# Optimization experiments

Hardware: AMD Instinct MI355X
Metric: run time of the kernel (lower is better)

The kernel has to match this reference:

```python
import jax, jax.numpy as jnp
import numpy as np

NUM_EXPERTS = 16
TOP_K = 2
FFT_LEN = 512
SEQ_LEN = 512
PRED_LEN = 720
MOE_TEMP = 1.0


def setup_inputs() -> dict:
    key = jax.random.key(0)
    ks = jax.random.split(key, 5)
    x = jax.random.normal(ks[0], (8192, SEQ_LEN), dtype=jnp.float32)
    # gating network: Linear(fft_len//2 -> num_experts)
    gw = jax.random.normal(ks[1], (NUM_EXPERTS, FFT_LEN // 2), dtype=jnp.float32) * (1.0 / np.sqrt(FFT_LEN // 2))
    gb = jnp.zeros((NUM_EXPERTS,), dtype=jnp.float32)
    # experts: RLinear = instance-norm (RevIN) + Linear(seq->pred), stacked
    ew = jax.random.normal(ks[2], (NUM_EXPERTS, SEQ_LEN, PRED_LEN), dtype=jnp.float32) * (1.0 / np.sqrt(SEQ_LEN))
    eb = jnp.zeros((NUM_EXPERTS, PRED_LEN), dtype=jnp.float32)
    return {"x": x, "gw": gw, "gb": gb, "ew": ew, "eb": eb}


def periodogram(x, n):
    # x: [B, L] -> normalized power spectrum [B, n//2]
    x0 = x - jnp.mean(x, axis=1, keepdims=True)
    dft = jnp.fft.fft(x0, n=n, axis=1) / jnp.sqrt(jnp.asarray(n, x.dtype))
    I = jnp.abs(dft[:, : n // 2]) ** 2
    s = jnp.sum(I, axis=1, keepdims=True)
    s = jnp.where(s == 0, 1.0, s)
    return I / s


def expert_apply(x, ew, eb):
    # RLinear: instance normalize, linear map, de-normalize
    mu = jnp.mean(x, axis=1, keepdims=True)
    sd = jnp.std(x, axis=1, keepdims=True) + 1e-5
    xn = (x - mu) / sd  # [B, L]
    # all experts densely: [B,L] x [E,L,P] -> [E,B,P]
    y = jnp.einsum('bl,elp->ebp', xn, ew) + eb[:, None, :]
    return y * sd[None] + mu[None]  # [E, B, P]


def reference(x, gw, gb, ew, eb):
    I = periodogram(x, FFT_LEN)  # [B, n//2]
    gate = (I @ gw.T + gb) / MOE_TEMP  # eval mode: divide by temp, no noise
    topk_vals, topk_idx = jax.lax.top_k(gate, TOP_K)  # [B, k]
    gates = jax.nn.softmax(topk_vals, axis=1)  # [B, k]
    expert_out = expert_apply(x, ew, eb)  # [E, B, P]
    # gather selected experts: [B, k, P]
    sel = jnp.take_along_axis(
        jnp.transpose(expert_out, (1, 0, 2)), topk_idx[:, :, None], axis=1
    )
    return jnp.sum(gates[:, :, None] * sel, axis=1)  # [B, P]
```

## Files before the change

kernel.cpp:

```cpp
#include <hip/hip_runtime.h>
#include <hip/hip_bf16.h>
#include <math.h>

#define NEXP  16
#define SEQ   512
#define PRED  720
#define NROWS 8192
#define NFREQ 256

typedef __bf16 bf16x8 __attribute__((ext_vector_type(8)));
typedef float  f32x16 __attribute__((ext_vector_type(16)));

__device__ __forceinline__ void gload_lds16(const void* g, void* l) {
    __builtin_amdgcn_global_load_lds(
        (const __attribute__((address_space(1))) unsigned int*)g,
        (__attribute__((address_space(3))) unsigned int*)l, 16, 0, 0);
}

__device__ __forceinline__ int xcd_swizzle(int bid, int nwg) {
    const int q = nwg >> 3, r = nwg & 7;
    const int xcd = bid & 7, off = bid >> 3;
    return (xcd < r ? xcd * (q + 1) : r * (q + 1) + (xcd - r) * q) + off;
}

__global__ __launch_bounds__(256) void k_preproc(const float* __restrict__ ew,
                                                 const float* __restrict__ x,
                                                 __hip_bfloat16* __restrict__ ewt,
                                                 __hip_bfloat16* __restrict__ bthi,
                                                 __hip_bfloat16* __restrict__ btlo,
                                                 __hip_bfloat16* __restrict__ xn,
                                                 __hip_bfloat16* __restrict__ xnlo,
                                                 float* __restrict__ meta,
                                                 int* __restrict__ nredo)
{
    const int bid = blockIdx.x;
    const int t   = threadIdx.x;

    if (bid < 512) {
        if (bid == 0 && t == 0) *nredo = 0;
        const int tid  = bid * 256 + t;
        const int f    = tid >> 9;
        const int lidx = tid & 511;
        const int m    = (f * lidx) & 511;

        constexpr double Cj[9] = {0.9999247018391445033, 0.9996988186962042201,
                                  0.9987954562051723927, 0.9951847266721968862,
                                  0.9807852804032304491, 0.9238795325112867561,
                                  0.7071067811865475244, 0.0, -1.0};
        constexpr double Sj[9] = {0.0122715382857199261, 0.0245412285229122880,
                                  0.0490676743274180143, 0.0980171403295606020,
                                  0.1950903220161282678, 0.3826834323650897717,
                                  0.7071067811865475244, 1.0, 0.0};
        double cr = 1.0, ci = 0.0;
#pragma unroll
        for (int j = 0; j < 9; ++j) {
            const bool on = (m >> j) & 1;
            const double mr = on ? Cj[j] : 1.0;
            const double mi = on ? Sj[j] : 0.0;
            const double nr = cr * mr - ci * mi;
            ci = cr * mi + ci * mr;
            cr = nr;
        }
        const size_t c0 = (size_t)(2 * f) * 512 + lidx;
        const size_t c1 = (size_t)(2 * f + 1) * 512 + lidx;
        {
            __hip_bfloat16 h = __float2bfloat16((float)cr);
            float hif = __bfloat162float(h);
            bthi[c0] = h;
            btlo[c0] = __float2bfloat16((float)(cr - (double)hif));
        }
        {
            __hip_bfloat16 h = __float2bfloat16((float)ci);
            float hif = __bfloat162float(h);
            bthi[c1] = h;
            btlo[c1] = __float2bfloat16((float)(ci - (double)hif));
        }
        return;
    }

    if (bid < 6400) {
        __shared__ float tile[32][33];
        const int rel = bid - 512;
        const int e   = rel / 368;
        const int rem = rel % 368;
        const int p0  = (rem % 23) * 32;
        const int l0  = (rem / 23) * 32;
        const int tx  = t & 31;
        const int ty  = t >> 5;
        const float* src = ew + (size_t)e * SEQ * PRED;
#pragma unroll
        for (int i = 0; i < 4; ++i) {
            int l = l0 + ty + i * 8;
            int p = p0 + tx;
            tile[ty + i * 8][tx] = (p < PRED) ? src[(size_t)l * PRED + p] : 0.f;
        }
        __syncthreads();
        __hip_bfloat16* dst = ewt + (size_t)e * PRED * SEQ;
#pragma unroll
        for (int i = 0; i < 4; ++i) {
            int p = p0 + ty + i * 8;
            int l = l0 + tx;
            if (p < PRED) dst[(size_t)p * SEQ + l] = __float2bfloat16(tile[tx][ty + i * 8]);
        }
        return;
    }

    {
        const int wv = t >> 6, l = t & 63;
        const int b  = (bid - 6400) * 4 + wv;
        const float* xr = x + (size_t)b * SEQ;

        const float4 v0 = *(const float4*)(xr + l * 8);
        const float4 v1 = *(const float4*)(xr + l * 8 + 4);
        const double d0 = v0.x, d1 = v0.y, d2 = v0.z, d3 = v0.w;
        const double d4 = v1.x, d5 = v1.y, d6 = v1.z, d7 = v1.w;

        double s1 = ((d0 + d1) + (d2 + d3)) + ((d4 + d5) + (d6 + d7));
        double s2 = ((d0 * d0 + d1 * d1) + (d2 * d2 + d3 * d3)) +
                    ((d4 * d4 + d5 * d5) + (d6 * d6 + d7 * d7));
#pragma unroll
        for (int off = 1; off < 64; off <<= 1) {
            s1 += __shfl_xor(s1, off);
            s2 += __shfl_xor(s2, off);
        }
        const double mu = s1 * (1.0 / 512.0);
        double var = s2 * (1.0 / 512.0) - mu * mu;
        if (var < 0.0) var = 0.0;
        const double sd = sqrt(var) + 1e-5, inv = 1.0 / sd;

        unsigned int hw[4], lw[4];
#define CONV(j, dj)                                                         \
        {                                                                   \
            double xnd = (dj - mu) * inv;                                   \
            __hip_bfloat16 h = __float2bfloat16((float)xnd);                \
            float hif = __bfloat162float(h);                                \
            __hip_bfloat16 lo = __float2bfloat16((float)(xnd - (double)hif)); \
            unsigned int hb = *(unsigned short*)&h;                         \
            unsigned int lb = *(unsigned short*)&lo;                        \
            if ((j & 1) == 0) { hw[j >> 1] = hb; lw[j >> 1] = lb; }         \
            else { hw[j >> 1] |= hb << 16; lw[j >> 1] |= lb << 16; }        \
        }
        CONV(0, d0) CONV(1, d1) CONV(2, d2) CONV(3, d3)
        CONV(4, d4) CONV(5, d5) CONV(6, d6) CONV(7, d7)
#undef CONV
        *(uint4*)(xn   + (size_t)b * SEQ + l * 8) = uint4{hw[0], hw[1], hw[2], hw[3]};
        *(uint4*)(xnlo + (size_t)b * SEQ + l * 8) = uint4{lw[0], lw[1], lw[2], lw[3]};

        if (l == 0) {
            meta[b * 4 + 0] = (float)mu;
            meta[b * 4 + 3] = (float)sd;
        }
    }
}

__global__ __launch_bounds__(256, 3) void k_dft_gemm(
    const __hip_bfloat16* __restrict__ xn, const __hip_bfloat16* __restrict__ xnlo,
    const __hip_bfloat16* __restrict__ bthi, const __hip_bfloat16* __restrict__ btlo,
    float* __restrict__ Iout)
{
    const int wgid = xcd_swizzle(blockIdx.x, 1024);
    const int rt = wgid >> 3;
    const int ct = wgid & 7;

    __shared__ __align__(16) __hip_bfloat16 As[3][64][64];
    __shared__ __align__(16) __hip_bfloat16 Bs[3][64][64];

    const int t  = threadIdx.x;
    const int wv = t >> 6, l = t & 63;

    size_t aoff[2], boff[2];
    int ldsrow[2], ldschk[2];
#pragma unroll
    for (int i = 0; i < 2; ++i) {
        const int idx = i * 256 + t;
        const int row = idx >> 3, chk = idx & 7;
        const int swz = (row & 7) ^ ((row & 8) >> 1);
        ldsrow[i] = row; ldschk[i] = chk;
        aoff[i] = (size_t)(rt * 64 + row) * SEQ + (size_t)(chk ^ swz) * 8;
        boff[i] = (size_t)(ct * 64 + row) * SEQ + (size_t)(chk ^ swz) * 8;
    }

#define DSTAGE(buf, kk) do {                                                   \
    const int pass_ = (kk) >> 3;                                               \
    const int koff_ = ((kk) & 7) * 64;                                         \
    const __hip_bfloat16* ap_ = (pass_ == 1) ? xnlo : xn;                      \
    const __hip_bfloat16* bp_ = (pass_ == 2) ? btlo : bthi;                    \
    _Pragma("unroll")                                                          \
    for (int i_ = 0; i_ < 2; ++i_)                                             \
        gload_lds16(ap_ + aoff[i_] + koff_, &As[buf][ldsrow[i_]][ldschk[i_] * 8]); \
    _Pragma("unroll")                                                          \
    for (int i_ = 0; i_ < 2; ++i_)                                             \
        gload_lds16(bp_ + boff[i_] + koff_, &Bs[buf][ldsrow[i_]][ldschk[i_] * 8]); \
} while (0)

    f32x16 acc;
#pragma unroll
    for (int q = 0; q < 16; ++q) acc[q] = 0.f;

    const int wr = wv >> 1, wc = wv & 1;
    const int fl = l & 31, fh = l >> 5;
    const int rswz = (fl & 7) ^ ((fl & 8) >> 1);

    DSTAGE(0, 0);
    DSTAGE(1, 1);
#pragma unroll
    for (int kt = 0; kt < 24; ++kt) {
        const int cur = kt % 3;
        if (kt < 23) asm volatile("s_waitcnt vmcnt(4)" ::: "memory");
        else         asm volatile("s_waitcnt vmcnt(0)" ::: "memory");
        __builtin_amdgcn_sched_barrier(0);
        __builtin_amdgcn_s_barrier();
        __builtin_amdgcn_sched_barrier(0);
#pragma unroll
        for (int ks = 0; ks < 4; ++ks) {
            const int cc = ((ks * 2 + fh) ^ rswz) * 8;
            const bf16x8 a = *(const bf16x8*)&As[cur][wr * 32 + fl][cc];
            const bf16x8 b = *(const bf16x8*)&Bs[cur][wc * 32 + fl][cc];
            acc = __builtin_amdgcn_mfma_f32_32x32x16_bf16(a, b, acc, 0, 0, 0);
        }
        if (kt + 2 < 24) DSTAGE((kt + 2) % 3, kt + 2);
    }
#undef DSTAGE

    const int crow_base = 4 * fh;
    const int col = ct * 64 + wc * 32 + fl;
#pragma unroll
    for (int q = 0; q < 16; ++q) {
        const float v = acc[q];
        const float w = __shfl_xor(v, 1);
        if ((fl & 1) == 0) {
            const int rl = wr * 32 + (q & 3) + 8 * (q >> 2) + crow_base;
            Iout[(size_t)(rt * 64 + rl) * NFREQ + (col >> 1)] = v * v + w * w;
        }
    }
}

__global__ __launch_bounds__(256) void k_gatefin(const float* __restrict__ Iout,
                                                 const float* __restrict__ gw,
                                                 const float* __restrict__ gb,
                                                 float* __restrict__ meta,
                                                 int* __restrict__ eidx,
                                                 int* __restrict__ redo,
                                                 int* __restrict__ nredo)
{
    __shared__ float gws[NEXP * 257];
    __shared__ float Pw[4][256];
    __shared__ float Gs[4][16];

    const int t  = threadIdx.x;
    const int wv = t >> 6, l = t & 63;
    const int b  = blockIdx.x * 4 + wv;

    for (int i = t; i < NEXP * NFREQ; i += 256)
        gws[(i >> 8) * 257 + (i & 255)] = gw[i];
    __syncthreads();

    const float* Ir = Iout + (size_t)b * NFREQ;
    const float i0 = Ir[l], i1 = Ir[64 + l], i2 = Ir[128 + l], i3 = Ir[192 + l];
    Pw[wv][l] = i0; Pw[wv][64 + l] = i1; Pw[wv][128 + l] = i2; Pw[wv][192 + l] = i3;
    float ps = (i0 + i1) + (i2 + i3);
#pragma unroll
    for (int off = 1; off < 64; off <<= 1) ps += __shfl_xor(ps, off);

    const int e = l >> 2, kb = l & 3;
    float acc = 0.f;
#pragma unroll 8
    for (int j = 0; j < 64; ++j) {
        const int k = kb + 4 * j;
        acc += Pw[wv][k] * gws[e * 257 + k];
    }
    acc += __shfl_xor(acc, 1);
    acc += __shfl_xor(acc, 2);
    if (kb == 0) Gs[wv][e] = acc;

    if (l == 0) {
        const float sdiv  = (ps == 0.f) ? 1.f : ps;
        const float inv_s = 1.f / sdiv;
        float b1 = -1e30f, b2 = -1e30f, b3 = -1e30f;
        int i1b = 0, i2b = 0;
#pragma unroll
        for (int i = 0; i < NEXP; ++i) {
            float v = Gs[wv][i] * inv_s + gb[i];
            if (v > b1)      { b3 = b2; b2 = b1; i2b = i1b; b1 = v; i1b = i; }
            else if (v > b2) { b3 = b2; b2 = v; i2b = i; }
            else if (v > b3) { b3 = v; }
        }
        if (b2 - b3 < 1e-4f * fmaxf(1.f, fabsf(b1))) {
            const int r = atomicAdd(nredo, 1);
            redo[r] = b;
        } else {
            const float sd = meta[b * 4 + 3];
            const float ee = __expf(b2 - b1);
            const float w0 = 1.f / (1.f + ee);
            const float w1 = ee / (1.f + ee);
            meta[b * 4 + 1] = w0 * sd;
            meta[b * 4 + 2] = w1 * sd;
            eidx[b * 2 + 0] = i1b;
            eidx[b * 2 + 1] = i2b;
        }
    }
}

__global__ __launch_bounds__(256, 4) void k_gate64(const float* __restrict__ x,
                                                   const float* __restrict__ gw,
                                                   const float* __restrict__ gb,
                                                   float* __restrict__ meta,
                                                   int* __restrict__ eidx,
                                                   const int* __restrict__ redo,
                                                   const int* __restrict__ nredo)
{
    __shared__ double Pw[4][256];
    __shared__ double Gs[4][16];

    const int t  = threadIdx.x;
    const int wv = t >> 6, l = t & 63;
    const int n  = *nredo;

    for (int it = blockIdx.x * 4 + wv; it < n; it += gridDim.x * 4) {
        const int b = redo[it];
        const float* xr = x + (size_t)b * SEQ;

        double s1 = 0.0, s2 = 0.0;
#define DLOADV(n_) double vr##n_ = (double)xr[64 * n_ + l]; s1 += vr##n_; s2 += vr##n_ * vr##n_;
        DLOADV(0) DLOADV(1) DLOADV(2) DLOADV(3) DLOADV(4) DLOADV(5) DLOADV(6) DLOADV(7)
#undef DLOADV
        double vi0, vi1, vi2, vi3, vi4, vi5, vi6, vi7;

#pragma unroll
        for (int off = 1; off < 64; off <<= 1) {
            s1 += __shfl_xor(s1, off);
            s2 += __shfl_xor(s2, off);
        }
        const double mu = s1 * (1.0 / 512.0);
        double var = s2 * (1.0 / 512.0) - mu * mu;
        if (var < 0.0) var = 0.0;
        const double sd = sqrt(var) + 1e-5;

#define DSUB(n_) vr##n_ -= mu;
        DSUB(0) DSUB(1) DSUB(2) DSUB(3) DSUB(4) DSUB(5) DSUB(6) DSUB(7)
#undef DSUB

        {
            const double C = 0.70710678118654752440084436210485;
            double a0 = vr0 + vr4, a1 = vr1 + vr5, a2 = vr2 + vr6, a3 = vr3 + vr7;
            double d0 = vr0 - vr4, d1 = vr1 - vr5, d2 = vr2 - vr6, d3 = vr3 - vr7;
            double c0 = a0 + a2, c2 = a0 - a2, c1 = a1 + a3;
            double c3i = a3 - a1;
            double e1r = C * (d1 - d3), e1i = -C * (d1 + d3);
            vr0 = c0 + c1;   vi0 = 0.0;
            vr1 = c0 - c1;   vi1 = 0.0;
            vr2 = c2;        vi2 = c3i;
            vr3 = c2;        vi3 = -c3i;
            vr4 = d0 + e1r;  vi4 = -d2 + e1i;
            vr5 = d0 - e1r;  vi5 = -d2 - e1i;
            vr6 = d0 - e1r;  vi6 =  d2 + e1i;
            vr7 = d0 + e1r;  vi7 =  d2 - e1i;
        }

        double w1r = 1.0, w1i = 0.0;
        {
            constexpr double Cr[6] = {0.9999247018391445033, 0.9996988186962042201,
                                      0.9987954562051723927, 0.9951847266721968862,
                                      0.9807852804032304491, 0.9238795325112867561};
            constexpr double Ci[6] = {-0.0122715382857199261, -0.0245412285229122880,
                                      -0.0490676743274180143, -0.0980171403295606020,
                                      -0.1950903220161282678, -0.3826834323650897717};
#pragma unroll
            for (int j = 0; j < 6; ++j) {
                const bool on = (l >> j) & 1;
                const double mr = on ? Cr[j] : 1.0;
                const double mi = on ? Ci[j] : 0.0;
                const double nr = w1r * mr - w1i * mi;
                w1i = w1r * mi + w1i * mr;
                w1r = nr;
            }
        }

        {
            double wkr = w1r, wki = w1i;
#define DTWID(n_) { double tr_ = vr##n_ * wkr - vi##n_ * wki; \
                    vi##n_ = vr##n_ * wki + vi##n_ * wkr; vr##n_ = tr_; }
#define DWSTEP() { double nr_ = wkr * w1r - wki * w1i; \
                   wki = wkr * w1i + wki * w1r; wkr = nr_; }
            DTWID(4) DWSTEP() DTWID(2) DWSTEP() DTWID(6) DWSTEP() DTWID(1)
            DWSTEP() DTWID(5) DWSTEP() DTWID(3) DWSTEP() DTWID(7)
#undef DTWID
#undef DWSTEP
        }

        double twr, twi;
        {
            double w2r = w1r * w1r - w1i * w1i, w2i = 2.0 * w1r * w1i;
            double w4r = w2r * w2r - w2i * w2i, w4i = 2.0 * w2r * w2i;
            twr = w4r * w4r - w4i * w4i; twi = 2.0 * w4r * w4i;
        }
#define DBF(R, I, h, hi, ter, tei) { \
        double br_ = __shfl_xor(R, h); double bi_ = __shfl_xor(I, h); \
        double dr_ = hi ? (R - br_) : (R + br_); \
        double di_ = hi ? (I - bi_) : (I + bi_); \
        R = dr_ * ter - di_ * tei; I = dr_ * tei + di_ * ter; }
#define DSTG(hc) { \
        const bool hi_ = (l & hc) != 0; \
        const double ter_ = hi_ ? twr : 1.0; \
        const double tei_ = hi_ ? twi : 0.0; \
        DBF(vr0, vi0, hc, hi_, ter_, tei_) DBF(vr1, vi1, hc, hi_, ter_, tei_) \
        DBF(vr2, vi2, hc, hi_, ter_, tei_) DBF(vr3, vi3, hc, hi_, ter_, tei_) \
        DBF(vr4, vi4, hc, hi_, ter_, tei_) DBF(vr5, vi5, hc, hi_, ter_, tei_) \
        DBF(vr6, vi6, hc, hi_, ter_, tei_) DBF(vr7, vi7, hc, hi_, ter_, tei_) \
        double ntr_ = twr * twr - twi * twi; twi = 2.0 * twr * twi; twr = ntr_; }
        DSTG(32) DSTG(16) DSTG(8) DSTG(4) DSTG(2) DSTG(1)
#undef DSTG
#undef DBF

        const int k2 = (int)(__brev((unsigned)l) >> 26);
        double ps = 0.0;
        if ((l & 1) == 0) {
            const int kb = 8 * k2;
            double P;
            P = vr0 * vr0 + vi0 * vi0; ps += P; Pw[wv][0 + kb] = P;
            P = vr1 * vr1 + vi1 * vi1; ps += P; Pw[wv][4 + kb] = P;
            P = vr2 * vr2 + vi2 * vi2; ps += P; Pw[wv][2 + kb] = P;
            P = vr3 * vr3 + vi3 * vi3; ps += P; Pw[wv][6 + kb] = P;
            P = vr4 * vr4 + vi4 * vi4; ps += P; Pw[wv][1 + kb] = P;
            P = vr5 * vr5 + vi5 * vi5; ps += P; Pw[wv][5 + kb] = P;
            P = vr6 * vr6 + vi6 * vi6; ps += P; Pw[wv][3 + kb] = P;
            P = vr7 * vr7 + vi7 * vi7; ps += P; Pw[wv][7 + kb] = P;
        }
#pragma unroll
        for (int off = 1; off < 64; off <<= 1) ps += __shfl_xor(ps, off);

        {
            const int e = l >> 2, kb = l & 3;
            double acc = 0.0;
#pragma unroll 8
            for (int j = 0; j < 64; ++j) {
                int k = kb + 4 * j;
                acc += Pw[wv][k] * (double)gw[e * NFREQ + k];
            }
            acc += __shfl_xor(acc, 1);
            acc += __shfl_xor(acc, 2);
            if (kb == 0) Gs[wv][e] = acc;
        }

        if (l == 0) {
            const double sdiv  = (ps == 0.0) ? 1.0 : ps;
            const double inv_s = 1.0 / sdiv;
            double best = -1e300, best2 = -1e300;
            int i0b = 0, i1b = 0;
#pragma unroll
            for (int i = 0; i < NEXP; ++i) {
                double v = Gs[wv][i] * inv_s + (double)gb[i];
                if (v > best)       { best2 = best; i1b = i0b; best = v; i0b = i; }
                else if (v > best2) { best2 = v; i1b = i; }
            }
            const double eexp = (double)__expf((float)(best2 - best));
            const double w0 = 1.0 / (1.0 + eexp);
            const double w1 = eexp / (1.0 + eexp);
            meta[b * 4 + 0] = (float)mu;
            meta[b * 4 + 1] = (float)(w0 * sd);
            meta[b * 4 + 2] = (float)(w1 * sd);
            meta[b * 4 + 3] = (float)sd;
            eidx[b * 2 + 0] = i0b;
            eidx[b * 2 + 1] = i1b;
        }
    }
}

__global__ __launch_bounds__(256) void k_count(const int* __restrict__ eidx,
                                               int* __restrict__ blockHist)
{
    __shared__ int h[32];
    const int t   = threadIdx.x;
    const int blk = blockIdx.x;
    if (t < 32) h[t] = 0;
    __syncthreads();
    const int b  = blk * 256 + t;
    const int e0 = eidx[2 * b];
    const int e1 = eidx[2 * b + 1];
    atomicAdd(&h[e0], 1);
    atomicAdd(&h[16 + e1], 1);
    __syncthreads();
    if (t < 32) blockHist[(t >> 4) * 512 + blk * 16 + (t & 15)] = h[t];
}

__global__ void k_scan(const int* __restrict__ blockHist, int* __restrict__ counts,
                       int* __restrict__ offs, int* __restrict__ tdesc,
                       int* __restrict__ base)
{
    __shared__ int cnt[32];
    __shared__ int off_s[32];
    const int j = threadIdx.x;
    if (j < 32) {
        const int s = j >> 4, e = j & 15;
        int acc = 0;
        for (int blk = 0; blk < 32; ++blk) acc += blockHist[s * 512 + blk * 16 + e];
        cnt[j] = acc;
        counts[j] = acc;
    }
    __syncthreads();
    if (j < 2) {
        int acc = 0, tt = 0;
        for (int i = 0; i < NEXP; ++i) {
            const int c = cnt[j * 16 + i];
            off_s[j * 16 + i] = acc;
            offs[j * 16 + i]  = acc;
            acc += c;
            const int nt = (c + 63) >> 6;
            for (int k = 0; k < nt; ++k) tdesc[j * 160 + tt++] = (i << 16) | k;
        }
        for (; tt < 160; ++tt) tdesc[j * 160 + tt] = -1;
    }
    __syncthreads();
    if (j < 32) {
        const int s = j >> 4, e = j & 15;
        int run = off_s[j];
        for (int blk = 0; blk < 32; ++blk) {
            base[s * 512 + blk * 16 + e] = run;
            run += blockHist[s * 512 + blk * 16 + e];
        }
    }
}

__global__ __launch_bounds__(256) void k_scatter(const int* __restrict__ eidx,
                                                 const int* __restrict__ base,
                                                 int* __restrict__ lists)
{
    __shared__ int whist[2][4][16];
    const int t   = threadIdx.x;
    const int wv  = t >> 6, l = t & 63;
    const int blk = blockIdx.x;
    const int b   = blk * 256 + t;
    const int e0  = eidx[2 * b];
    const int e1  = eidx[2 * b + 1];
    const unsigned long long before = (1ULL << l) - 1ULL;

    unsigned long long m0 = 0, m1 = 0;
#pragma unroll
    for (int bb = 0; bb < 16; ++bb) {
        unsigned long long m = __ballot(e0 == bb);
        if (e0 == bb) m0 = m;
        if (l == 0) whist[0][wv][bb] = __popcll(m);
    }
#pragma unroll
    for (int bb = 0; bb < 16; ++bb) {
        unsigned long long m = __ballot(e1 == bb);
        if (e1 == bb) m1 = m;
        if (l == 0) whist[1][wv][bb] = __popcll(m);
    }
    __syncthreads();

    int p0 = __popcll(m0 & before);
    int p1 = __popcll(m1 & before);
    for (int w = 0; w < 4; ++w) {
        if (w < wv) {
            p0 += whist[0][w][e0];
            p1 += whist[1][w][e1];
        }
    }
    lists[base[blk * 16 + e0] + p0]                 = b;
    lists[NROWS + base[512 + blk * 16 + e1] + p1]   = b;
}

__global__ __launch_bounds__(256, 3) void k_expert_gemm(
    const __hip_bfloat16* __restrict__ xn, const __hip_bfloat16* __restrict__ ewt,
    const float* __restrict__ eb, const float* __restrict__ meta,
    const int* __restrict__ lists, const int* __restrict__ offs,
    const int* __restrict__ counts, const int* __restrict__ tdesc,
    float* __restrict__ out, float* __restrict__ out2)
{
    const int wgid = xcd_swizzle(blockIdx.x, 3456);
    const int slot = wgid / 1728;
    const int rem  = wgid - slot * 1728;
    const int tid  = rem / 12;
    const int ct   = rem % 12;
    const int d    = tdesc[slot * 160 + tid];
    if (d < 0) return;
    const int e  = d >> 16;
    const int rt = d & 0xffff;
    const int n_e = counts[slot * NEXP + e];

    __shared__ __align__(16) __hip_bfloat16 As[3][64][64];
    __shared__ __align__(16) __hip_bfloat16 Bs[3][64][64];
    __shared__ int   rowB[64];
    __shared__ float rowMu[64];
    __shared__ float rowC[64];

    const int t  = threadIdx.x;
    const int wv = t >> 6, l = t & 63;
    const int* list = lists + slot * NROWS + offs[slot * NEXP + e];
    if (t < 64) {
        int r  = rt * 64 + t;
        int bb = (r < n_e) ? list[r] : -1;
        rowB[t]  = bb;
        rowMu[t] = (bb >= 0) ? meta[bb * 4] : 0.f;
        rowC[t]  = (bb >= 0) ? meta[bb * 4 + 1 + slot] : 0.f;
    }
    __syncthreads();

    const __hip_bfloat16* asrc[2];
    const __hip_bfloat16* bsrc[2];
    int ldsrow[2], ldschk[2];
#pragma unroll
    for (int i = 0; i < 2; ++i) {
        const int idx = i * 256 + t;
        const int row = idx >> 3, chk = idx & 7;
        const int swz = (row & 7) ^ ((row & 8) >> 1);
        ldsrow[i] = row; ldschk[i] = chk;
        const int ab  = rowB[row];
        asrc[i] = xn + ((ab >= 0) ? (size_t)ab * SEQ : 0) + (size_t)(chk ^ swz) * 8;
        const int gc  = ct * 64 + row;
        const int gcc = (gc < PRED) ? gc : (PRED - 1);
        bsrc[i] = ewt + ((size_t)e * PRED + gcc) * SEQ + (size_t)(chk ^ swz) * 8;
    }

#define STAGE(buf, koff) do {                                                      \
    _Pragma("unroll")                                                              \
    for (int i_ = 0; i_ < 2; ++i_)                                                 \
        gload_lds16(asrc[i_] + (koff), &As[buf][ldsrow[i_]][ldschk[i_] * 8]);      \
    _Pragma("unroll")                                                              \
    for (int i_ = 0; i_ < 2; ++i_)                                                 \
        gload_lds16(bsrc[i_] + (koff), &Bs[buf][ldsrow[i_]][ldschk[i_] * 8]);      \
} while (0)

    f32x16 acc;
#pragma unroll
    for (int q = 0; q < 16; ++q) acc[q] = 0.f;

    const int wr = wv >> 1, wc = wv & 1;
    const int fl = l & 31, fh = l >> 5;
    const int rswz = (fl & 7) ^ ((fl & 8) >> 1);

    STAGE(0, 0);
    STAGE(1, 64);
#pragma unroll
    for (int kt = 0; kt < 8; ++kt) {
        const int cur = kt % 3;
        if (kt < 7) asm volatile("s_waitcnt vmcnt(4)" ::: "memory");
        else        asm volatile("s_waitcnt vmcnt(0)" ::: "memory");
        __builtin_amdgcn_sched_barrier(0);
        __builtin_amdgcn_s_barrier();
        __builtin_amdgcn_sched_barrier(0);
#pragma unroll
        for (int ks = 0; ks < 4; ++ks) {
            const int cc = ((ks * 2 + fh) ^ rswz) * 8;
            const bf16x8 a = *(const bf16x8*)&As[cur][wr * 32 + fl][cc];
            const bf16x8 b = *(const bf16x8*)&Bs[cur][wc * 32 + fl][cc];
            acc = __builtin_amdgcn_mfma_f32_32x32x16_bf16(a, b, acc, 0, 0, 0);
        }
        if (kt + 2 < 8) STAGE((kt + 2) % 3, (kt + 2) * 64);
    }
#undef STAGE

    const int crow_base = 4 * fh;
    const int col = ct * 64 + wc * 32 + fl;
    const bool cok = (col < PRED);
    const float ebv = cok ? eb[e * PRED + col] : 0.f;
#pragma unroll
    for (int q = 0; q < 16; ++q) {
        const int rl = wr * 32 + (q & 3) + 8 * (q >> 2) + crow_base;
        const int bb = rowB[rl];
        if (!cok || bb < 0) continue;
        const float v = acc[q] + ebv;
        if (slot == 0) out [(size_t)bb * PRED + col] = rowMu[rl] + rowC[rl] * v;
        else           out2[(size_t)bb * PRED + col] = rowC[rl] * v;
    }
}

__global__ __launch_bounds__(256) void k_merge(float* __restrict__ out,
                                               const float* __restrict__ out2)
{
    const int i = blockIdx.x * 256 + threadIdx.x;
    float4 a = ((float4*)out)[i];
    const float4 b = ((const float4*)out2)[i];
    a.x += b.x; a.y += b.y; a.z += b.z; a.w += b.w;
    ((float4*)out)[i] = a;
}

extern "C" void kernel_launch(void* const* d_in, const int* in_sizes, int n_in,
                              void* d_out, int out_size, void* d_ws, size_t ws_size,
                              hipStream_t stream)
{
    const float* x  = (const float*)d_in[0];
    const float* gw = (const float*)d_in[1];
    const float* gb = (const float*)d_in[2];
    const float* ew = (const float*)d_in[3];
    const float* eb = (const float*)d_in[4];
    float* out = (float*)d_out;
    char*  ws  = (char*)d_ws;

    constexpr size_t XN_OFF   = 0;
    constexpr size_t XN_SZ    = (size_t)NROWS * SEQ * 2;
    constexpr size_t XNLO_OFF = XN_OFF + XN_SZ;
    constexpr size_t EWT_OFF  = XNLO_OFF + XN_SZ;
    constexpr size_t EWT_SZ   = (size_t)NEXP * PRED * SEQ * 2;
    constexpr size_t BTHI_OFF = EWT_OFF + EWT_SZ;
    constexpr size_t BT_SZ    = (size_t)512 * 512 * 2;
    constexpr size_t BTLO_OFF = BTHI_OFF + BT_SZ;
    constexpr size_t IOUT_OFF = BTLO_OFF + BT_SZ;
    constexpr size_t IOUT_SZ  = (size_t)NROWS * NFREQ * 4;
    constexpr size_t META_OFF = IOUT_OFF + IOUT_SZ;
    constexpr size_t META_SZ  = (size_t)NROWS * 4 * 4;
    constexpr size_t EIDX_OFF = META_OFF + META_SZ;
    constexpr size_t EIDX_SZ  = (size_t)NROWS * 2 * 4;
    constexpr size_t LIST_OFF = EIDX_OFF + EIDX_SZ;
    constexpr size_t LIST_SZ  = (size_t)2 * NROWS * 4;
    constexpr size_t CNT_OFF  = LIST_OFF + LIST_SZ;
    constexpr size_t OFFS_OFF = CNT_OFF + 144;
    constexpr size_t TDSC_OFF = OFFS_OFF + 128;
    constexpr size_t BH_OFF   = TDSC_OFF + 1280;
    constexpr size_t BASE_OFF = BH_OFF + 4096;
    constexpr size_t REDO_OFF = BASE_OFF + 4096;
    constexpr size_t OUT2_OFF = REDO_OFF + (size_t)NROWS * 4;

    __hip_bfloat16* xn   = (__hip_bfloat16*)(ws + XN_OFF);
    __hip_bfloat16* xnlo = (__hip_bfloat16*)(ws + XNLO_OFF);
    __hip_bfloat16* ewt  = (__hip_bfloat16*)(ws + EWT_OFF);
    __hip_bfloat16* bthi = (__hip_bfloat16*)(ws + BTHI_OFF);
    __hip_bfloat16* btlo = (__hip_bfloat16*)(ws + BTLO_OFF);
    float* Iout  = (float*)(ws + IOUT_OFF);
    float* meta  = (float*)(ws + META_OFF);
    int* eidx    = (int*)(ws + EIDX_OFF);
    int* lists   = (int*)(ws + LIST_OFF);
    int* counts  = (int*)(ws + CNT_OFF);
    int* nredo   = (int*)(ws + CNT_OFF + 128);
    int* offs    = (int*)(ws + OFFS_OFF);
    int* tdesc   = (int*)(ws + TDSC_OFF);
    int* bhist   = (int*)(ws + BH_OFF);
    int* base    = (int*)(ws + BASE_OFF);
    int* redo    = (int*)(ws + REDO_OFF);
    float* out2  = (float*)(ws + OUT2_OFF);

    k_preproc<<<dim3(8448), dim3(256), 0, stream>>>(ew, x, ewt, bthi, btlo,
                                                    xn, xnlo, meta, nredo);
    k_dft_gemm<<<dim3(1024), dim3(256), 0, stream>>>(xn, xnlo, bthi, btlo, Iout);
    k_gatefin<<<dim3(NROWS / 4), dim3(256), 0, stream>>>(Iout, gw, gb, meta, eidx,
                                                         redo, nredo);
    k_gate64<<<dim3(64), dim3(256), 0, stream>>>(x, gw, gb, meta, eidx, redo, nredo);
    k_count<<<dim3(32), dim3(256), 0, stream>>>(eidx, bhist);
    k_scan<<<dim3(1), dim3(64), 0, stream>>>(bhist, counts, offs, tdesc, base);
    k_scatter<<<dim3(32), dim3(256), 0, stream>>>(eidx, base, lists);
    k_expert_gemm<<<dim3(3456), dim3(256), 0, stream>>>(
        xn, ewt, eb, meta, lists, offs, counts, tdesc, out, out2);
    k_merge<<<dim3(NROWS * PRED / 1024), dim3(256), 0, stream>>>(out, out2);
}
```

Measured before the change: 141.7 us.

## Widen GEMM N-tiles to 128 with double buffering and MFMA priority boost

```diff
diff --git a/kernel.cpp b/kernel.cpp
--- a/kernel.cpp
+++ b/kernel.cpp
@@ -158,26 +158,33 @@
     const __hip_bfloat16* __restrict__ bthi, const __hip_bfloat16* __restrict__ btlo,
     float* __restrict__ Iout)
 {
-    const int wgid = xcd_swizzle(blockIdx.x, 1024);
-    const int rt = wgid >> 3;
-    const int ct = wgid & 7;
-
-    __shared__ __align__(16) __hip_bfloat16 As[3][64][64];
-    __shared__ __align__(16) __hip_bfloat16 Bs[3][64][64];
+    const int wgid = xcd_swizzle(blockIdx.x, 512);
+    const int rt = wgid >> 2;
+    const int ct = wgid & 3;
+
+    __shared__ __align__(16) __hip_bfloat16 As[2][64][64];
+    __shared__ __align__(16) __hip_bfloat16 Bs[2][128][64];
 
     const int t  = threadIdx.x;
     const int wv = t >> 6, l = t & 63;
 
-    size_t aoff[2], boff[2];
-    int ldsrow[2], ldschk[2];
+    size_t aoff[2], boff[4];
+    int arow[2], achk[2], brow[4], bchk[4];
 #pragma unroll
     for (int i = 0; i < 2; ++i) {
         const int idx = i * 256 + t;
         const int row = idx >> 3, chk = idx & 7;
         const int swz = (row & 7) ^ ((row & 8) >> 1);
-        ldsrow[i] = row; ldschk[i] = chk;
+        arow[i] = row; achk[i] = chk;
         aoff[i] = (size_t)(rt * 64 + row) * SEQ + (size_t)(chk ^ swz) * 8;
-        boff[i] = (size_t)(ct * 64 + row) * SEQ + (size_t)(chk ^ swz) * 8;
+    }
+#pragma unroll
+    for (int i = 0; i < 4; ++i) {
+        const int idx = i * 256 + t;
+        const int row = idx >> 3, chk = idx & 7;
+        const int swz = (row & 7) ^ ((row & 8) >> 1);
+        brow[i] = row; bchk[i] = chk;
+        boff[i] = (size_t)(ct * 128 + row) * SEQ + (size_t)(chk ^ swz) * 8;
     }
 
 #define DSTAGE(buf, kk) do {                                                   \
@@ -187,50 +194,59 @@
     const __hip_bfloat16* bp_ = (pass_ == 2) ? btlo : bthi;                    \
     _Pragma("unroll")                                                          \
     for (int i_ = 0; i_ < 2; ++i_)                                             \
-        gload_lds16(ap_ + aoff[i_] + koff_, &As[buf][ldsrow[i_]][ldschk[i_] * 8]); \
+        gload_lds16(ap_ + aoff[i_] + koff_, &As[buf][arow[i_]][achk[i_] * 8]); \
     _Pragma("unroll")                                                          \
-    for (int i_ = 0; i_ < 2; ++i_)                                             \
-        gload_lds16(bp_ + boff[i_] + koff_, &Bs[buf][ldsrow[i_]][ldschk[i_] * 8]); \
+    for (int i_ = 0; i_ < 4; ++i_)                                             \
+        gload_lds16(bp_ + boff[i_] + koff_, &Bs[buf][brow[i_]][bchk[i_] * 8]); \
 } while (0)
 
-    f32x16 acc;
-#pragma unroll
-    for (int q = 0; q < 16; ++q) acc[q] = 0.f;
+    f32x16 acc[2];
+#pragma unroll
+    for (int ni = 0; ni < 2; ++ni)
+#pragma unroll
+        for (int q = 0; q < 16; ++q) acc[ni][q] = 0.f;
 
     const int wr = wv >> 1, wc = wv & 1;
     const int fl = l & 31, fh = l >> 5;
     const int rswz = (fl & 7) ^ ((fl & 8) >> 1);
 
     DSTAGE(0, 0);
-    DSTAGE(1, 1);
+    asm volatile("s_waitcnt vmcnt(0)" ::: "memory");
+    __builtin_amdgcn_s_barrier();
 #pragma unroll
     for (int kt = 0; kt < 24; ++kt) {
-        const int cur = kt % 3;
-        if (kt < 23) asm volatile("s_waitcnt vmcnt(4)" ::: "memory");
-        else         asm volatile("s_waitcnt vmcnt(0)" ::: "memory");
+        const int cur = kt & 1;
+        if (kt < 23) DSTAGE(cur ^ 1, kt + 1);
         __builtin_amdgcn_sched_barrier(0);
-        __builtin_amdgcn_s_barrier();
-        __builtin_amdgcn_sched_barrier(0);
+        __builtin_amdgcn_s_setprio(1);
 #pragma unroll
         for (int ks = 0; ks < 4; ++ks) {
             const int cc = ((ks * 2 + fh) ^ rswz) * 8;
-            const bf16x8 a = *(const bf16x8*)&As[cur][wr * 32 + fl][cc];
-            const bf16x8 b = *(const bf16x8*)&Bs[cur][wc * 32 + fl][cc];
-            acc = __builtin_amdgcn_mfma_f32_32x32x16_bf16(a, b, acc, 0, 0, 0);
-        }
-        if (kt + 2 < 24) DSTAGE((kt + 2) % 3, kt + 2);
+            const bf16x8 a  = *(const bf16x8*)&As[cur][wr * 32 + fl][cc];
+            const bf16x8 b0 = *(const bf16x8*)&Bs[cur][wc * 64 + fl][cc];
+            const bf16x8 b1 = *(const bf16x8*)&Bs[cur][wc * 64 + 32 + fl][cc];
+            acc[0] = __builtin_amdgcn_mfma_f32_32x32x16_bf16(a, b0, acc[0], 0, 0, 0);
+            acc[1] = __builtin_amdgcn_mfma_f32_32x32x16_bf16(a, b1, acc[1], 0, 0, 0);
+        }
+        __builtin_amdgcn_s_setprio(0);
+        __builtin_amdgcn_sched_barrier(0);
+        asm volatile("s_waitcnt vmcnt(0)" ::: "memory");
+        __builtin_amdgcn_s_barrier();
     }
 #undef DSTAGE
 
     const int crow_base = 4 * fh;
-    const int col = ct * 64 + wc * 32 + fl;
-#pragma unroll
-    for (int q = 0; q < 16; ++q) {
-        const float v = acc[q];
-        const float w = __shfl_xor(v, 1);
-        if ((fl & 1) == 0) {
-            const int rl = wr * 32 + (q & 3) + 8 * (q >> 2) + crow_base;
-            Iout[(size_t)(rt * 64 + rl) * NFREQ + (col >> 1)] = v * v + w * w;
+#pragma unroll
+    for (int ni = 0; ni < 2; ++ni) {
+        const int col = ct * 128 + wc * 64 + ni * 32 + fl;
+#pragma unroll
+        for (int q = 0; q < 16; ++q) {
+            const float v = acc[ni][q];
+            const float w = __shfl_xor(v, 1);
+            if ((fl & 1) == 0) {
+                const int rl = wr * 32 + (q & 3) + 8 * (q >> 2) + crow_base;
+                Iout[(size_t)(rt * 64 + rl) * NFREQ + (col >> 1)] = v * v + w * w;
+            }
         }
     }
 }
@@ -568,19 +584,19 @@
     const int* __restrict__ counts, const int* __restrict__ tdesc,
     float* __restrict__ out, float* __restrict__ out2)
 {
-    const int wgid = xcd_swizzle(blockIdx.x, 3456);
-    const int slot = wgid / 1728;
-    const int rem  = wgid - slot * 1728;
-    const int tid  = rem / 12;
-    const int ct   = rem % 12;
+    const int wgid = xcd_swizzle(blockIdx.x, 1920);
+    const int slot = wgid / 960;
+    const int rem  = wgid - slot * 960;
+    const int tid  = rem / 6;
+    const int ct   = rem % 6;
     const int d    = tdesc[slot * 160 + tid];
     if (d < 0) return;
     const int e  = d >> 16;
     const int rt = d & 0xffff;
     const int n_e = counts[slot * NEXP + e];
 
-    __shared__ __align__(16) __hip_bfloat16 As[3][64][64];
-    __shared__ __align__(16) __hip_bfloat16 Bs[3][64][64];
+    __shared__ __align__(16) __hip_bfloat16 As[2][64][64];
+    __shared__ __align__(16) __hip_bfloat16 Bs[2][128][64];
     __shared__ int   rowB[64];
     __shared__ float rowMu[64];
     __shared__ float rowC[64];
@@ -598,71 +614,87 @@
     __syncthreads();
 
     const __hip_bfloat16* asrc[2];
-    const __hip_bfloat16* bsrc[2];
-    int ldsrow[2], ldschk[2];
+    const __hip_bfloat16* bsrc[4];
+    int arow[2], achk[2], brow[4], bchk[4];
 #pragma unroll
     for (int i = 0; i < 2; ++i) {
         const int idx = i * 256 + t;
         const int row = idx >> 3, chk = idx & 7;
         const int swz = (row & 7) ^ ((row & 8) >> 1);
-        ldsrow[i] = row; ldschk[i] = chk;
-        const int ab  = rowB[row];
+        arow[i] = row; achk[i] = chk;
+        const int ab = rowB[row];
         asrc[i] = xn + ((ab >= 0) ? (size_t)ab * SEQ : 0) + (size_t)(chk ^ swz) * 8;
-        const int gc  = ct * 64 + row;
+    }
+#pragma unroll
+    for (int i = 0; i < 4; ++i) {
+        const int idx = i * 256 + t;
+        const int row = idx >> 3, chk = idx & 7;
+        const int swz = (row & 7) ^ ((row & 8) >> 1);
+        brow[i] = row; bchk[i] = chk;
+        const int gc  = ct * 128 + row;
         const int gcc = (gc < PRED) ? gc : (PRED - 1);
         bsrc[i] = ewt + ((size_t)e * PRED + gcc) * SEQ + (size_t)(chk ^ swz) * 8;
     }
 
-#define STAGE(buf, koff) do {                                                      \
-    _Pragma("unroll")                                                              \
-    for (int i_ = 0; i_ < 2; ++i_)                                                 \
-        gload_lds16(asrc[i_] + (koff), &As[buf][ldsrow[i_]][ldschk[i_] * 8]);      \
-    _Pragma("unroll")                                                              \
-    for (int i_ = 0; i_ < 2; ++i_)                                                 \
-        gload_lds16(bsrc[i_] + (koff), &Bs[buf][ldsrow[i_]][ldschk[i_] * 8]);      \
+#define STAGE(buf, koff) do {                                                  \
+    _Pragma("unroll")                                                          \
+    for (int i_ = 0; i_ < 2; ++i_)                                             \
+        gload_lds16(asrc[i_] + (koff), &As[buf][arow[i_]][achk[i_] * 8]);      \
+    _Pragma("unroll")                                                          \
+    for (int i_ = 0; i_ < 4; ++i_)                                             \
+        gload_lds16(bsrc[i_] + (koff), &Bs[buf][brow[i_]][bchk[i_] * 8]);      \
 } while (0)
 
-    f32x16 acc;
-#pragma unroll
-    for (int q = 0; q < 16; ++q) acc[q] = 0.f;
+    f32x16 acc[2];
+#pragma unroll
+    for (int ni = 0; ni < 2; ++ni)
+#pragma unroll
+        for (int q = 0; q < 16; ++q) acc[ni][q] = 0.f;
 
     const int wr = wv >> 1, wc = wv & 1;
     const int fl = l & 31, fh = l >> 5;
     const int rswz = (fl & 7) ^ ((fl & 8) >> 1);
 
     STAGE(0, 0);
-    STAGE(1, 64);
+    asm volatile("s_waitcnt vmcnt(0)" ::: "memory");
+    __builtin_amdgcn_s_barrier();
 #pragma unroll
     for (int kt = 0; kt < 8; ++kt) {
-        const int cur = kt % 3;
-        if (kt < 7) asm volatile("s_waitcnt vmcnt(4)" ::: "memory");
-        else        asm volatile("s_waitcnt vmcnt(0)" ::: "memory");
+        const int cur = kt & 1;
+        if (kt < 7) STAGE(cur ^ 1, (kt + 1) * 64);
         __builtin_amdgcn_sched_barrier(0);
-        __builtin_amdgcn_s_barrier();
-        __builtin_amdgcn_sched_barrier(0);
+        __builtin_amdgcn_s_setprio(1);
 #pragma unroll
         for (int ks = 0; ks < 4; ++ks) {
             const int cc = ((ks * 2 + fh) ^ rswz) * 8;
-            const bf16x8 a = *(const bf16x8*)&As[cur][wr * 32 + fl][cc];
-            const bf16x8 b = *(const bf16x8*)&Bs[cur][wc * 32 + fl][cc];
-            acc = __builtin_amdgcn_mfma_f32_32x32x16_bf16(a, b, acc, 0, 0, 0);
-        }
-        if (kt + 2 < 8) STAGE((kt + 2) % 3, (kt + 2) * 64);
+            const bf16x8 a  = *(const bf16x8*)&As[cur][wr * 32 + fl][cc];
+            const bf16x8 b0 = *(const bf16x8*)&Bs[cur][wc * 64 + fl][cc];
+            const bf16x8 b1 = *(const bf16x8*)&Bs[cur][wc * 64 + 32 + fl][cc];
+            acc[0] = __builtin_amdgcn_mfma_f32_32x32x16_bf16(a, b0, acc[0], 0, 0, 0);
+            acc[1] = __builtin_amdgcn_mfma_f32_32x32x16_bf16(a, b1, acc[1], 0, 0, 0);
+        }
+        __builtin_amdgcn_s_setprio(0);
+        __builtin_amdgcn_sched_barrier(0);
+        asm volatile("s_waitcnt vmcnt(0)" ::: "memory");
+        __builtin_amdgcn_s_barrier();
     }
 #undef STAGE
 
     const int crow_base = 4 * fh;
-    const int col = ct * 64 + wc * 32 + fl;
-    const bool cok = (col < PRED);
-    const float ebv = cok ? eb[e * PRED + col] : 0.f;
-#pragma unroll
-    for (int q = 0; q < 16; ++q) {
-        const int rl = wr * 32 + (q & 3) + 8 * (q >> 2) + crow_base;
-        const int bb = rowB[rl];
-        if (!cok || bb < 0) continue;
-        const float v = acc[q] + ebv;
-        if (slot == 0) out [(size_t)bb * PRED + col] = rowMu[rl] + rowC[rl] * v;
-        else           out2[(size_t)bb * PRED + col] = rowC[rl] * v;
+#pragma unroll
+    for (int ni = 0; ni < 2; ++ni) {
+        const int col = ct * 128 + wc * 64 + ni * 32 + fl;
+        const bool cok = (col < PRED);
+        const float ebv = cok ? eb[e * PRED + col] : 0.f;
+#pragma unroll
+        for (int q = 0; q < 16; ++q) {
+            const int rl = wr * 32 + (q & 3) + 8 * (q >> 2) + crow_base;
+            const int bb = rowB[rl];
+            if (!cok || bb < 0) continue;
+            const float v = acc[ni][q] + ebv;
+            if (slot == 0) out [(size_t)bb * PRED + col] = rowMu[rl] + rowC[rl] * v;
+            else           out2[(size_t)bb * PRED + col] = rowC[rl] * v;
+        }
     }
 }
 
@@ -732,14 +764,14 @@
 
     k_preproc<<<dim3(8448), dim3(256), 0, stream>>>(ew, x, ewt, bthi, btlo,
                                                     xn, xnlo, meta, nredo);
-    k_dft_gemm<<<dim3(1024), dim3(256), 0, stream>>>(xn, xnlo, bthi, btlo, Iout);
+    k_dft_gemm<<<dim3(512), dim3(256), 0, stream>>>(xn, xnlo, bthi, btlo, Iout);
     k_gatefin<<<dim3(NROWS / 4), dim3(256), 0, stream>>>(Iout, gw, gb, meta, eidx,
                                                          redo, nredo);
     k_gate64<<<dim3(64), dim3(256), 0, stream>>>(x, gw, gb, meta, eidx, redo, nredo);
     k_count<<<dim3(32), dim3(256), 0, stream>>>(eidx, bhist);
     k_scan<<<dim3(1), dim3(64), 0, stream>>>(bhist, counts, offs, tdesc, base);
     k_scatter<<<dim3(32), dim3(256), 0, stream>>>(eidx, base, lists);
-    k_expert_gemm<<<dim3(3456), dim3(256), 0, stream>>>(
+    k_expert_gemm<<<dim3(1920), dim3(256), 0, stream>>>(
         xn, ewt, eb, meta, lists, offs, counts, tdesc, out, out2);
     k_merge<<<dim3(NROWS * PRED / 1024), dim3(256), 0, stream>>>(out, out2);
 }
```

New measurement: 141.4 us. No clear change (-0.2%).
